# Kernel optimization log

Hardware: AMD Instinct MI355X
Metric: run time of the kernel (lower is better)

Reference implementation:

```python
import jax, jax.numpy as jnp
import numpy as np

EMBED = 1024
HEAD = 128

def setup_inputs() -> dict:
    key = jax.random.key(0)
    k1, k2, k3, k4 = jax.random.split(key, 4)
    x = jax.random.normal(k1, (8, 2048, EMBED), dtype=jnp.float32)
    s = 1.0 / np.sqrt(EMBED)
    Wk = jax.random.normal(k2, (EMBED, HEAD), dtype=jnp.float32) * s
    Wq = jax.random.normal(k3, (EMBED, HEAD), dtype=jnp.float32) * s
    Wv = jax.random.normal(k4, (EMBED, HEAD), dtype=jnp.float32) * s
    return {"x": x, "Wk": Wk, "Wq": Wq, "Wv": Wv}

def reference(x, Wk, Wq, Wv):
    # x: [B,T,E]; projections: [B,T,H]
    k = x @ Wk
    q = x @ Wq
    v = x @ Wv
    T = x.shape[1]
    # NOTE: original scales by 1/sqrt(embedding_size), not head_size
    scale = 1.0 / jnp.sqrt(jnp.asarray(EMBED, dtype=x.dtype))
    scores = jnp.einsum('bth,bsh->bts', q, k) * scale  # [B,T,T]
    causal = jnp.tril(jnp.ones((T, T), dtype=bool))
    scores = jnp.where(causal, scores, -jnp.inf)
    attn = jax.nn.softmax(scores, axis=-1)
    return jnp.einsum('bts,bsh->bth', attn, v)
```

## Files before the change

### kernel.cpp

```cpp
#include <hip/hip_runtime.h>
#include <math.h>

typedef short bf16x2 __attribute__((ext_vector_type(2)));
typedef short bf16x4 __attribute__((ext_vector_type(4)));
typedef short bf16x8 __attribute__((ext_vector_type(8)));
typedef float f32x4 __attribute__((ext_vector_type(4)));

#define EMBED 1024
#define HEAD 128
#define BATCH 8
#define SEQ 2048

__device__ __forceinline__ short f2bf(float f) {
  union { float f; unsigned u; } v;
  v.f = f;
  unsigned r = v.u + 0x7fffu + ((v.u >> 16) & 1u);
  return (short)(r >> 16);
}

__device__ __forceinline__ void async_copy16(const void* g, void* l) {
#if __has_builtin(__builtin_amdgcn_global_load_lds)
  __builtin_amdgcn_global_load_lds(
      (const __attribute__((address_space(1))) unsigned int*)g,
      (__attribute__((address_space(3))) unsigned int*)l, 16, 0, 0);
#else
  *(f32x4*)l = *(const f32x4*)g;
#endif
}

__global__ __launch_bounds__(384) void wtrans_kernel(
    const float* __restrict__ Wq, const float* __restrict__ Wk,
    const float* __restrict__ Wv, short* __restrict__ WT3) {
  int kc8 = blockIdx.x;
  int n = threadIdx.x;
  int mtx = n >> 7, h = n & 127;
  const float* W = (mtx == 0) ? Wq : ((mtx == 1) ? Wk : Wv);
  float scale = (mtx == 0) ? (1.4426950408889634f / 32.0f) : 1.0f;
  bf16x8 o;
#pragma unroll
  for (int j = 0; j < 8; j++)
    o[j] = f2bf(W[(size_t)(kc8 * 8 + j) * HEAD + h] * scale);
  *(bf16x8*)&WT3[(size_t)kc8 * 3072 + n * 8] = o;
}

__global__ __launch_bounds__(512, 2) void proj_kernel(
    const float* __restrict__ x, const short* __restrict__ WT3,
    short* __restrict__ q, short* __restrict__ kG, short* __restrict__ vG) {
  __shared__ __align__(16) short As[2][64 * 72];
  __shared__ __align__(16) short Bs[2][24576];
  int tid = threadIdx.x;
  int w = tid >> 6, lane = tid & 63, quad = lane >> 4, sub = lane & 15;
  int mw = w & 1, nw = w >> 1;
  int mt = blockIdx.x;
  int m0 = mt * 64;

  int arow = tid >> 3;
  int akq = (tid & 7) * 8;
  const float* xbase = x + (size_t)(m0 + arow) * EMBED + akq;
  int aoff = arow * 72 + akq;

  int kcg = tid >> 7;
  int n0 = tid & 127;
  int bdst[6];
#pragma unroll
  for (int j = 0; j < 3; j++)
#pragma unroll
    for (int kk = 0; kk < 2; kk++)
      bdst[j * 2 + kk] = ((kcg * 2 + kk) * 384 + j * 128 + n0) * 8;

  f32x4 acc[2][6];
#pragma unroll
  for (int am = 0; am < 2; am++)
#pragma unroll
    for (int an = 0; an < 6; an++) acc[am][an] = (f32x4)(0.0f);

  {
    f32x4 x0 = *(const f32x4*)(xbase + 0);
    f32x4 x1 = *(const f32x4*)(xbase + 4);
    bf16x8 w0;
    w0[0]=f2bf(x0[0]); w0[1]=f2bf(x0[1]); w0[2]=f2bf(x0[2]); w0[3]=f2bf(x0[3]);
    w0[4]=f2bf(x1[0]); w0[5]=f2bf(x1[1]); w0[6]=f2bf(x1[2]); w0[7]=f2bf(x1[3]);
    *(bf16x8*)&As[0][aoff] = w0;
#pragma unroll
    for (int j = 0; j < 6; j++) async_copy16(WT3 + bdst[j], &Bs[0][bdst[j]]);
  }
  f32x4 xr0 = *(const f32x4*)(xbase + 64);
  f32x4 xr1 = *(const f32x4*)(xbase + 68);

  for (int it = 0; it < 16; it++) {
    int cur = it & 1;
    __syncthreads();
    if (it < 15) {
      int nxt = cur ^ 1;
      bf16x8 w0;
      w0[0]=f2bf(xr0[0]); w0[1]=f2bf(xr0[1]); w0[2]=f2bf(xr0[2]); w0[3]=f2bf(xr0[3]);
      w0[4]=f2bf(xr1[0]); w0[5]=f2bf(xr1[1]); w0[6]=f2bf(xr1[2]); w0[7]=f2bf(xr1[3]);
      *(bf16x8*)&As[nxt][aoff] = w0;
      int bsrc = (it + 1) * 24576;
#pragma unroll
      for (int j = 0; j < 6; j++)
        async_copy16(WT3 + bsrc + bdst[j], &Bs[nxt][bdst[j]]);
      if (it < 14) {
        int kb2 = (it + 2) * 64;
        xr0 = *(const f32x4*)(xbase + kb2);
        xr1 = *(const f32x4*)(xbase + kb2 + 4);
      }
    }
#pragma unroll
    for (int ks = 0; ks < 2; ks++) {
      bf16x8 a0 = *(const bf16x8*)&As[cur][(mw * 32 + sub) * 72 + ks * 32 + quad * 8];
      bf16x8 a1 = *(const bf16x8*)&As[cur][(mw * 32 + 16 + sub) * 72 + ks * 32 + quad * 8];
#pragma unroll
      for (int an = 0; an < 6; an++) {
        bf16x8 bf = *(const bf16x8*)&Bs[cur][((ks * 4 + quad) * 384 + nw * 96 + an * 16 + sub) * 8];
        acc[0][an] = __builtin_amdgcn_mfma_f32_16x16x32_bf16(a0, bf, acc[0][an], 0, 0, 0);
        acc[1][an] = __builtin_amdgcn_mfma_f32_16x16x32_bf16(a1, bf, acc[1][an], 0, 0, 0);
      }
    }
  }

#pragma unroll
  for (int am = 0; am < 2; am++)
#pragma unroll
    for (int an = 0; an < 6; an++) {
      int g = nw * 6 + an;
      int hcol = (g & 7) * 16 + sub;
      if (g < 8) {
#pragma unroll
        for (int r = 0; r < 4; r++) {
          int m = m0 + mw * 32 + am * 16 + quad * 4 + r;
          q[(size_t)m * HEAD + hcol] = f2bf(acc[am][an][r]);
        }
      } else if (g < 16) {
        size_t base = (size_t)(mt * 2 + mw) * 4096 + (hcol >> 3) * 256 + (hcol & 7);
#pragma unroll
        for (int r = 0; r < 4; r++)
          kG[base + (am * 16 + quad * 4 + r) * 8] = f2bf(acc[am][an][r]);
      } else {
        bf16x4 pv;
#pragma unroll
        for (int r = 0; r < 4; r++) pv[r] = f2bf(acc[am][an][r]);
        *(bf16x4*)&vG[(size_t)(mt * 2 + mw) * 4096 + (am * 2 + (quad >> 1)) * 1024 +
                      hcol * 8 + (quad & 1) * 4] = pv;
      }
    }
}

__global__ __launch_bounds__(256, 4) void attn_kernel(
    const short* __restrict__ q, const short* __restrict__ kG,
    const short* __restrict__ vG, float* __restrict__ o_acc,
    float* __restrict__ l_acc) {
  __shared__ __align__(16) short Kb[2][4096];
  __shared__ __align__(16) short Vb[2][4096];
  __shared__ __align__(16) short Pb[4][2][16 * 40];
  int tid = threadIdx.x;
  int w = tid >> 6, lane = tid & 63, quad = lane >> 4, sub = lane & 15;
  int bx = blockIdx.x;
  int b = bx & 7;
  int v = 79 - (bx >> 3);
  int qt, c;
  if (v < 8)       { qt = v;                               c = 0; }
  else if (v < 24) { int i2 = v - 8;  qt = 8  + (i2 >> 1); c = i2 & 1; }
  else if (v < 48) { int i2 = v - 24; qt = 16 + i2 / 3;    c = i2 % 3; }
  else             { int i2 = v - 48; qt = 24 + (i2 >> 2); c = i2 & 3; }
  int q0 = qt * 64;
  int kb0 = c * 512;
  int len = min(512, q0 + 64 - kb0);
  int ntiles = len >> 5;

  const short* kp = kG + (size_t)b * SEQ * HEAD;
  const short* vp = vG + (size_t)b * SEQ * HEAD;
  int cc0 = tid, cc1 = tid + 256;

  bf16x8 qf[4];
  const short* qrow = q + (size_t)(b * SEQ + q0 + w * 16 + sub) * HEAD + quad * 8;
#pragma unroll
  for (int kc = 0; kc < 4; kc++) qf[kc] = *(const bf16x8*)(qrow + kc * 32);

  f32x4 o[8];
#pragma unroll
  for (int h = 0; h < 8; h++) o[h] = (f32x4)(0.0f);
  float l[4] = {0.0f, 0.0f, 0.0f, 0.0f};
  int wrow = q0 + w * 16;
  int qrq = wrow + quad * 4;

  {
    size_t blk = (size_t)(kb0 >> 5) * 4096;
    async_copy16(kp + blk + cc0 * 8, &Kb[0][cc0 * 8]);
    async_copy16(kp + blk + cc1 * 8, &Kb[0][cc1 * 8]);
    async_copy16(vp + blk + cc0 * 8, &Vb[0][cc0 * 8]);
    async_copy16(vp + blk + cc1 * 8, &Vb[0][cc1 * 8]);
  }

  for (int j = 0; j < ntiles; j++) {
    int kb = kb0 + j * 32;
    int cur = j & 1;
    __syncthreads();
    if (j + 1 < ntiles) {
      int nxt = cur ^ 1;
      size_t blk = (size_t)((kb + 32) >> 5) * 4096;
      async_copy16(kp + blk + cc0 * 8, &Kb[nxt][cc0 * 8]);
      async_copy16(kp + blk + cc1 * 8, &Kb[nxt][cc1 * 8]);
      async_copy16(vp + blk + cc0 * 8, &Vb[nxt][cc0 * 8]);
      async_copy16(vp + blk + cc1 * 8, &Vb[nxt][cc1 * 8]);
    }
    f32x4 s0 = (f32x4)(0.0f), s1 = (f32x4)(0.0f);
#pragma unroll
    for (int kk = 0; kk < 4; kk++) {
      bf16x8 f0 = *(const bf16x8*)&Kb[cur][((kk * 4 + quad) * 32 + sub) * 8];
      bf16x8 f1 = *(const bf16x8*)&Kb[cur][((kk * 4 + quad) * 32 + 16 + sub) * 8];
      s0 = __builtin_amdgcn_mfma_f32_16x16x32_bf16(qf[kk], f0, s0, 0, 0, 0);
      s1 = __builtin_amdgcn_mfma_f32_16x16x32_bf16(qf[kk], f1, s1, 0, 0, 0);
    }
    bool edge = (kb + 31 > wrow);
    float e0[4], e1[4];
#pragma unroll
    for (int r = 0; r < 4; r++) {
      e0[r] = __builtin_amdgcn_exp2f(s0[r]);
      e1[r] = __builtin_amdgcn_exp2f(s1[r]);
    }
    if (edge) {
#pragma unroll
      for (int r = 0; r < 4; r++) {
        if (kb + sub > qrq + r) e0[r] = 0.0f;
        if (kb + 16 + sub > qrq + r) e1[r] = 0.0f;
      }
    }
    short* pw = &Pb[w][cur][0];
#pragma unroll
    for (int r = 0; r < 4; r++) {
      l[r] += e0[r] + e1[r];
      pw[(quad * 4 + r) * 40 + sub] = f2bf(e0[r]);
      pw[(quad * 4 + r) * 40 + sub + 16] = f2bf(e1[r]);
    }
    bf16x8 pa = *(const bf16x8*)&pw[sub * 40 + quad * 8];
#pragma unroll
    for (int h8 = 0; h8 < 8; h8++) {
      bf16x8 vf = *(const bf16x8*)&Vb[cur][(quad * 128 + h8 * 16 + sub) * 8];
      o[h8] = __builtin_amdgcn_mfma_f32_16x16x32_bf16(pa, vf, o[h8], 0, 0, 0);
    }
  }

  float* ob = o_acc + (size_t)(b * SEQ + qrq) * HEAD + sub;
#pragma unroll
  for (int r = 0; r < 4; r++)
#pragma unroll
    for (int h8 = 0; h8 < 8; h8++)
      unsafeAtomicAdd(ob + (size_t)r * HEAD + h8 * 16, o[h8][r]);
#pragma unroll
  for (int r = 0; r < 4; r++) {
#pragma unroll
    for (int off = 1; off < 16; off <<= 1) l[r] += __shfl_xor(l[r], off);
  }
  if (sub == 0) {
#pragma unroll
    for (int r = 0; r < 4; r++)
      unsafeAtomicAdd(&l_acc[b * SEQ + qrq + r], l[r]);
  }
}

__global__ __launch_bounds__(256) void norm_kernel(
    float* __restrict__ o, const float* __restrict__ l_acc) {
  int idx = blockIdx.x * 256 + threadIdx.x;
  f32x4 v = ((const f32x4*)o)[idx];
  float inv = 1.0f / l_acc[idx >> 5];
  v[0] *= inv; v[1] *= inv; v[2] *= inv; v[3] *= inv;
  ((f32x4*)o)[idx] = v;
}

extern "C" void kernel_launch(void* const* d_in, const int* in_sizes, int n_in,
                              void* d_out, int out_size, void* d_ws, size_t ws_size,
                              hipStream_t stream) {
  const float* x  = (const float*)d_in[0];
  const float* Wk = (const float*)d_in[1];
  const float* Wq = (const float*)d_in[2];
  const float* Wv = (const float*)d_in[3];
  char* ws = (char*)d_ws;
  short* WT3   = (short*)(ws);
  short* vG    = (short*)(ws + (size_t)1  * (1 << 20));
  short* q     = (short*)(ws + (size_t)5  * (1 << 20));
  short* kG    = (short*)(ws + (size_t)9  * (1 << 20));
  float* l_acc = (float*)(ws + (size_t)13 * (1 << 20));
  float* out   = (float*)d_out;

  hipMemsetAsync(out, 0, (size_t)BATCH * SEQ * HEAD * sizeof(float), stream);
  hipMemsetAsync(l_acc, 0, (size_t)BATCH * SEQ * sizeof(float), stream);
  wtrans_kernel<<<dim3(128), 384, 0, stream>>>(Wq, Wk, Wv, WT3);
  proj_kernel<<<dim3(256), 512, 0, stream>>>(x, WT3, q, kG, vG);
  attn_kernel<<<dim3(640), 256, 0, stream>>>(q, kG, vG, out, l_acc);
  norm_kernel<<<dim3(2048), 256, 0, stream>>>(out, l_acc);
}
```

Measured before the change: 156.7 us.

## Triple-buffer K/V in attention with manual waitcnt barriers and MFMA priority

The attention kernel moves from double to triple buffering of K/V tiles, prefetching two tiles ahead, and replaces __syncthreads with explicit s_waitcnt vmcnt + s_barrier so outstanding async loads are not fully drained each iteration. MFMA sections are wrapped in s_setprio to favour matrix issue, and the P scratch buffer drops its double buffer. The projection kernel issues its weight async copies before the x conversion and waits on partial vmcnt. The aim is more memory latency hidden behind compute. In exchange, occupancy drops to 3 blocks per SM with more LDS, and the hand-written waitcnt counts must exactly match the outstanding loads, including the unconditional x loads, to stay correct.

```diff
diff --git a/kernel.cpp b/kernel.cpp
--- a/kernel.cpp
+++ b/kernel.cpp
@@ -89,22 +89,21 @@
 
   for (int it = 0; it < 16; it++) {
     int cur = it & 1;
-    __syncthreads();
+    asm volatile("s_waitcnt vmcnt(2) lgkmcnt(0)\n\ts_barrier" ::: "memory");
+    __builtin_amdgcn_sched_barrier(0);
     if (it < 15) {
       int nxt = cur ^ 1;
+      int bsrc = (it + 1) * 24576;
+#pragma unroll
+      for (int j = 0; j < 6; j++)
+        async_copy16(WT3 + bsrc + bdst[j], &Bs[nxt][bdst[j]]);
       bf16x8 w0;
       w0[0]=f2bf(xr0[0]); w0[1]=f2bf(xr0[1]); w0[2]=f2bf(xr0[2]); w0[3]=f2bf(xr0[3]);
       w0[4]=f2bf(xr1[0]); w0[5]=f2bf(xr1[1]); w0[6]=f2bf(xr1[2]); w0[7]=f2bf(xr1[3]);
       *(bf16x8*)&As[nxt][aoff] = w0;
-      int bsrc = (it + 1) * 24576;
-#pragma unroll
-      for (int j = 0; j < 6; j++)
-        async_copy16(WT3 + bsrc + bdst[j], &Bs[nxt][bdst[j]]);
-      if (it < 14) {
-        int kb2 = (it + 2) * 64;
-        xr0 = *(const f32x4*)(xbase + kb2);
-        xr1 = *(const f32x4*)(xbase + kb2 + 4);
-      }
+      int kb2 = (it < 14) ? (it + 2) * 64 : 0;
+      xr0 = *(const f32x4*)(xbase + kb2);
+      xr1 = *(const f32x4*)(xbase + kb2 + 4);
     }
 #pragma unroll
     for (int ks = 0; ks < 2; ks++) {
@@ -146,13 +145,13 @@
     }
 }
 
-__global__ __launch_bounds__(256, 4) void attn_kernel(
+__global__ __launch_bounds__(256, 3) void attn_kernel(
     const short* __restrict__ q, const short* __restrict__ kG,
     const short* __restrict__ vG, float* __restrict__ o_acc,
     float* __restrict__ l_acc) {
-  __shared__ __align__(16) short Kb[2][4096];
-  __shared__ __align__(16) short Vb[2][4096];
-  __shared__ __align__(16) short Pb[4][2][16 * 40];
+  __shared__ __align__(16) short Kb[3][4096];
+  __shared__ __align__(16) short Vb[3][4096];
+  __shared__ __align__(16) short Pb[4][16 * 40];
   int tid = threadIdx.x;
   int w = tid >> 6, lane = tid & 63, quad = lane >> 4, sub = lane & 15;
   int bx = blockIdx.x;
@@ -176,6 +175,12 @@
   const short* qrow = q + (size_t)(b * SEQ + q0 + w * 16 + sub) * HEAD + quad * 8;
 #pragma unroll
   for (int kc = 0; kc < 4; kc++) qf[kc] = *(const bf16x8*)(qrow + kc * 32);
+  {
+    int pin = 0;
+#pragma unroll
+    for (int kc = 0; kc < 4; kc++) pin += (int)qf[kc][0];
+    asm volatile("" :: "v"(pin));
+  }
 
   f32x4 o[8];
 #pragma unroll
@@ -190,21 +195,32 @@
     async_copy16(kp + blk + cc1 * 8, &Kb[0][cc1 * 8]);
     async_copy16(vp + blk + cc0 * 8, &Vb[0][cc0 * 8]);
     async_copy16(vp + blk + cc1 * 8, &Vb[0][cc1 * 8]);
+    blk += 4096;
+    async_copy16(kp + blk + cc0 * 8, &Kb[1][cc0 * 8]);
+    async_copy16(kp + blk + cc1 * 8, &Kb[1][cc1 * 8]);
+    async_copy16(vp + blk + cc0 * 8, &Vb[1][cc0 * 8]);
+    async_copy16(vp + blk + cc1 * 8, &Vb[1][cc1 * 8]);
   }
 
   for (int j = 0; j < ntiles; j++) {
     int kb = kb0 + j * 32;
-    int cur = j & 1;
-    __syncthreads();
+    int cur = j % 3;
     if (j + 1 < ntiles) {
-      int nxt = cur ^ 1;
-      size_t blk = (size_t)((kb + 32) >> 5) * 4096;
-      async_copy16(kp + blk + cc0 * 8, &Kb[nxt][cc0 * 8]);
-      async_copy16(kp + blk + cc1 * 8, &Kb[nxt][cc1 * 8]);
-      async_copy16(vp + blk + cc0 * 8, &Vb[nxt][cc0 * 8]);
-      async_copy16(vp + blk + cc1 * 8, &Vb[nxt][cc1 * 8]);
+      asm volatile("s_waitcnt vmcnt(4)\n\ts_barrier" ::: "memory");
+    } else {
+      asm volatile("s_waitcnt vmcnt(0)\n\ts_barrier" ::: "memory");
+    }
+    __builtin_amdgcn_sched_barrier(0);
+    if (j + 2 < ntiles) {
+      int nb = (j + 2) % 3;
+      size_t blk = (size_t)((kb + 64) >> 5) * 4096;
+      async_copy16(kp + blk + cc0 * 8, &Kb[nb][cc0 * 8]);
+      async_copy16(kp + blk + cc1 * 8, &Kb[nb][cc1 * 8]);
+      async_copy16(vp + blk + cc0 * 8, &Vb[nb][cc0 * 8]);
+      async_copy16(vp + blk + cc1 * 8, &Vb[nb][cc1 * 8]);
     }
     f32x4 s0 = (f32x4)(0.0f), s1 = (f32x4)(0.0f);
+    __builtin_amdgcn_s_setprio(1);
 #pragma unroll
     for (int kk = 0; kk < 4; kk++) {
       bf16x8 f0 = *(const bf16x8*)&Kb[cur][((kk * 4 + quad) * 32 + sub) * 8];
@@ -212,6 +228,7 @@
       s0 = __builtin_amdgcn_mfma_f32_16x16x32_bf16(qf[kk], f0, s0, 0, 0, 0);
       s1 = __builtin_amdgcn_mfma_f32_16x16x32_bf16(qf[kk], f1, s1, 0, 0, 0);
     }
+    __builtin_amdgcn_s_setprio(0);
     bool edge = (kb + 31 > wrow);
     float e0[4], e1[4];
 #pragma unroll
@@ -226,7 +243,7 @@
         if (kb + 16 + sub > qrq + r) e1[r] = 0.0f;
       }
     }
-    short* pw = &Pb[w][cur][0];
+    short* pw = &Pb[w][0];
 #pragma unroll
     for (int r = 0; r < 4; r++) {
       l[r] += e0[r] + e1[r];
@@ -234,11 +251,13 @@
       pw[(quad * 4 + r) * 40 + sub + 16] = f2bf(e1[r]);
     }
     bf16x8 pa = *(const bf16x8*)&pw[sub * 40 + quad * 8];
+    __builtin_amdgcn_s_setprio(1);
 #pragma unroll
     for (int h8 = 0; h8 < 8; h8++) {
       bf16x8 vf = *(const bf16x8*)&Vb[cur][(quad * 128 + h8 * 16 + sub) * 8];
       o[h8] = __builtin_amdgcn_mfma_f32_16x16x32_bf16(pa, vf, o[h8], 0, 0, 0);
     }
+    __builtin_amdgcn_s_setprio(0);
   }
 
   float* ob = o_acc + (size_t)(b * SEQ + qrq) * HEAD + sub;
```

Result: slower. 165.3 us (+5.5%).
